# Performance work log

Measured on AMD Instinct MI355X. Metric: run time of the kernel, lower is better.

## Reference

```python
import jax, jax.numpy as jnp
import numpy as np


def setup_inputs() -> dict:
    key = jax.random.key(0)
    k1, k2 = jax.random.split(key)
    x = jax.random.normal(k1, (128, 256, 32, 32), dtype=jnp.float32)
    T = jax.random.randint(k2, (128, 256, 1, 1), 0, 2, dtype=jnp.int32)
    return {"x": x, "T": T, "drop_block": 5}


def reference(x, T, drop_block):
    b, c, h, w = x.shape
    n = b * c
    xf = x.reshape(n, h, w)
    sel = (T.reshape(n) != 0)

    # per-slice argmax location
    flat = xf.reshape(n, h * w)
    max_index = jnp.argmax(flat, axis=1)
    mh = max_index // w
    mw = max_index % w

    half = int(np.floor(drop_block / 2.0))  # floor(drop_block/2)
    h1 = jnp.clip(mh - half, 0, h - 1)
    h2 = jnp.clip(mh + half, 0, h - 1)
    w1 = jnp.clip(mw - half, 0, w - 1)
    w2 = jnp.clip(mw + half, 0, w - 1)

    rows = jnp.arange(h)  # [h]
    cols = jnp.arange(w)  # [w]
    in_rows = (rows[None, :] >= h1[:, None]) & (rows[None, :] <= h2[:, None])  # [n,h]
    in_cols = (cols[None, :] >= w1[:, None]) & (cols[None, :] <= w2[:, None])  # [n,w]
    in_box = in_rows[:, :, None] & in_cols[:, None, :]                          # [n,h,w]
    S = 1.0 - in_box.astype(x.dtype)

    # normalization so expected activation magnitude is preserved
    lam = (h * w) / jnp.sum(S, axis=(1, 2))  # [n]
    masked = xf * S * lam[:, None, None]

    out = jnp.where(sel[:, None, None], masked, xf)
    return out.reshape(b, c, h, w)
```

## Files before the change

### kernel.cpp

```cpp
#include <hip/hip_runtime.h>

typedef float nfloat4 __attribute__((ext_vector_type(4)));

__global__ __launch_bounds__(256) void drop_block_kernel(
    const float* __restrict__ x,
    const int* __restrict__ T,
    const int* __restrict__ dropb,
    float* __restrict__ out,
    int n_slices) {
  const int wave_in_blk = threadIdx.x >> 6;
  const int lane = threadIdx.x & 63;
  const int slice = blockIdx.x * 4 + wave_in_blk;
  if (slice >= n_slices) return;

  const nfloat4* __restrict__ x4 = (const nfloat4*)x + (size_t)slice * 256;
  nfloat4* __restrict__ o4 = (nfloat4*)out + (size_t)slice * 256;

  nfloat4 v0 = __builtin_nontemporal_load(&x4[lane]);
  nfloat4 v1 = __builtin_nontemporal_load(&x4[lane + 64]);
  nfloat4 v2 = __builtin_nontemporal_load(&x4[lane + 128]);
  nfloat4 v3 = __builtin_nontemporal_load(&x4[lane + 192]);

  const int sel = T[slice];

  if (!sel) {
    __builtin_nontemporal_store(v0, &o4[lane]);
    __builtin_nontemporal_store(v1, &o4[lane + 64]);
    __builtin_nontemporal_store(v2, &o4[lane + 128]);
    __builtin_nontemporal_store(v3, &o4[lane + 192]);
    return;
  }

#define ARG4(vec, base, BV, BI)                         \
  float BV = vec.x; int BI = (base);                    \
  if (vec.y > BV) { BV = vec.y; BI = (base) + 1; }      \
  if (vec.z > BV) { BV = vec.z; BI = (base) + 2; }      \
  if (vec.w > BV) { BV = vec.w; BI = (base) + 3; }

  ARG4(v0, lane * 4, bv0, bi0)
  ARG4(v1, (lane + 64) * 4, bv1, bi1)
  ARG4(v2, (lane + 128) * 4, bv2, bi2)
  ARG4(v3, (lane + 192) * 4, bv3, bi3)
#undef ARG4

  float bv = bv0; int bi = bi0;
  if (bv1 > bv) { bv = bv1; bi = bi1; }
  if (bv2 > bv) { bv = bv2; bi = bi2; }
  if (bv3 > bv) { bv = bv3; bi = bi3; }

  for (int off = 32; off > 0; off >>= 1) {
    float ov = __shfl_xor(bv, off, 64);
    int oi = __shfl_xor(bi, off, 64);
    if (ov > bv || (ov == bv && oi < bi)) { bv = ov; bi = oi; }
  }

  const int half = dropb[0] >> 1;
  const int mh = bi >> 5;
  const int mw = bi & 31;
  int h1 = mh - half; h1 = h1 < 0 ? 0 : (h1 > 31 ? 31 : h1);
  int h2 = mh + half; h2 = h2 < 0 ? 0 : (h2 > 31 ? 31 : h2);
  int w1 = mw - half; w1 = w1 < 0 ? 0 : (w1 > 31 ? 31 : w1);
  int w2 = mw + half; w2 = w2 < 0 ? 0 : (w2 > 31 ? 31 : w2);
  const int area = (h2 - h1 + 1) * (w2 - w1 + 1);
  const float lam = 1024.0f / (float)(1024 - area);

#define APPLY(vec, base)                                              \
  do {                                                                \
    nfloat4 _r;                                                       \
    {                                                                 \
      int _i = (base);                                                \
      int _r0 = _i >> 5, _c0 = _i & 31;                               \
      bool _in = (_r0 >= h1) & (_r0 <= h2) & (_c0 >= w1) & (_c0 <= w2); \
      _r.x = _in ? 0.0f : vec.x * lam;                                \
      _c0 = (_i + 1) & 31; _r0 = (_i + 1) >> 5;                       \
      _in = (_r0 >= h1) & (_r0 <= h2) & (_c0 >= w1) & (_c0 <= w2);    \
      _r.y = _in ? 0.0f : vec.y * lam;                                \
      _c0 = (_i + 2) & 31; _r0 = (_i + 2) >> 5;                       \
      _in = (_r0 >= h1) & (_r0 <= h2) & (_c0 >= w1) & (_c0 <= w2);    \
      _r.z = _in ? 0.0f : vec.z * lam;                                \
      _c0 = (_i + 3) & 31; _r0 = (_i + 3) >> 5;                       \
      _in = (_r0 >= h1) & (_r0 <= h2) & (_c0 >= w1) & (_c0 <= w2);    \
      _r.w = _in ? 0.0f : vec.w * lam;                                \
    }                                                                 \
    __builtin_nontemporal_store(_r, &o4[(base) >> 2]);                \
  } while (0)

  APPLY(v0, lane * 4);
  APPLY(v1, (lane + 64) * 4);
  APPLY(v2, (lane + 128) * 4);
  APPLY(v3, (lane + 192) * 4);
#undef APPLY
}

extern "C" void kernel_launch(void* const* d_in, const int* in_sizes, int n_in,
                              void* d_out, int out_size, void* d_ws, size_t ws_size,
                              hipStream_t stream) {
  const float* x = (const float*)d_in[0];
  const int* T = (const int*)d_in[1];
  const int* dropb = (const int*)d_in[2];
  float* out = (float*)d_out;

  const int n_slices = in_sizes[1];
  const int blocks = (n_slices + 3) / 4;
  drop_block_kernel<<<blocks, 256, 0, stream>>>(x, T, dropb, out, n_slices);
}
```

Before: 220.8 us.

## Process two slices per wave and remove the unselected-slice branch

Each wavefront now handles two 32x32 slices, issuing eight vector loads up front, and interleaves the two argmax reductions. The separate early-exit copy path for unselected slices is removed: those slices go through the masking code with an empty box and a scale of one. Selection flags and the block size are read through readfirstlane so they live in scalar registers. The aim is more memory-level parallelism per wave and half as many blocks, at the cost of more registers and doing argmax work on slices that only need a copy.

```diff
diff --git a/kernel.cpp b/kernel.cpp
--- a/kernel.cpp
+++ b/kernel.cpp
@@ -8,28 +8,34 @@
     const int* __restrict__ dropb,
     float* __restrict__ out,
     int n_slices) {
-  const int wave_in_blk = threadIdx.x >> 6;
+  const int wave = threadIdx.x >> 6;
   const int lane = threadIdx.x & 63;
-  const int slice = blockIdx.x * 4 + wave_in_blk;
-  if (slice >= n_slices) return;
+  const int s0 = blockIdx.x * 8 + wave * 2;
+  if (s0 >= n_slices) return;
+  const bool has_b = (s0 + 1) < n_slices;
 
-  const nfloat4* __restrict__ x4 = (const nfloat4*)x + (size_t)slice * 256;
-  nfloat4* __restrict__ o4 = (nfloat4*)out + (size_t)slice * 256;
+  const nfloat4* __restrict__ xa = (const nfloat4*)x + (size_t)s0 * 256;
+  nfloat4* __restrict__ oa = (nfloat4*)out + (size_t)s0 * 256;
+  const nfloat4* __restrict__ xb = xa + 256;
+  nfloat4* __restrict__ ob = oa + 256;
 
-  nfloat4 v0 = __builtin_nontemporal_load(&x4[lane]);
-  nfloat4 v1 = __builtin_nontemporal_load(&x4[lane + 64]);
-  nfloat4 v2 = __builtin_nontemporal_load(&x4[lane + 128]);
-  nfloat4 v3 = __builtin_nontemporal_load(&x4[lane + 192]);
+  nfloat4 a0 = __builtin_nontemporal_load(&xa[lane]);
+  nfloat4 a1 = __builtin_nontemporal_load(&xa[lane + 64]);
+  nfloat4 a2 = __builtin_nontemporal_load(&xa[lane + 128]);
+  nfloat4 a3 = __builtin_nontemporal_load(&xa[lane + 192]);
+  nfloat4 b0, b1, b2, b3;
+  if (has_b) {
+    b0 = __builtin_nontemporal_load(&xb[lane]);
+    b1 = __builtin_nontemporal_load(&xb[lane + 64]);
+    b2 = __builtin_nontemporal_load(&xb[lane + 128]);
+    b3 = __builtin_nontemporal_load(&xb[lane + 192]);
+  } else {
+    b0 = a0; b1 = a1; b2 = a2; b3 = a3;
+  }
 
-  const int sel = T[slice];
-
-  if (!sel) {
-    __builtin_nontemporal_store(v0, &o4[lane]);
-    __builtin_nontemporal_store(v1, &o4[lane + 64]);
-    __builtin_nontemporal_store(v2, &o4[lane + 128]);
-    __builtin_nontemporal_store(v3, &o4[lane + 192]);
-    return;
-  }
+  int sel_a = __builtin_amdgcn_readfirstlane(T[s0]);
+  int sel_b = has_b ? __builtin_amdgcn_readfirstlane(T[s0 + 1]) : 0;
+  const int half = __builtin_amdgcn_readfirstlane(dropb[0]) >> 1;
 
 #define ARG4(vec, base, BV, BI)                         \
   float BV = vec.x; int BI = (base);                    \
@@ -37,58 +43,82 @@
   if (vec.z > BV) { BV = vec.z; BI = (base) + 2; }      \
   if (vec.w > BV) { BV = vec.w; BI = (base) + 3; }
 
-  ARG4(v0, lane * 4, bv0, bi0)
-  ARG4(v1, (lane + 64) * 4, bv1, bi1)
-  ARG4(v2, (lane + 128) * 4, bv2, bi2)
-  ARG4(v3, (lane + 192) * 4, bv3, bi3)
+  ARG4(a0, lane * 4, av0, ai0)
+  ARG4(a1, (lane + 64) * 4, av1, ai1)
+  ARG4(a2, (lane + 128) * 4, av2, ai2)
+  ARG4(a3, (lane + 192) * 4, av3, ai3)
+  ARG4(b0, lane * 4, bv0, bi0)
+  ARG4(b1, (lane + 64) * 4, bv1, bi1)
+  ARG4(b2, (lane + 128) * 4, bv2, bi2)
+  ARG4(b3, (lane + 192) * 4, bv3, bi3)
 #undef ARG4
 
+  float av = av0; int ai = ai0;
+  if (av1 > av) { av = av1; ai = ai1; }
+  if (av2 > av) { av = av2; ai = ai2; }
+  if (av3 > av) { av = av3; ai = ai3; }
   float bv = bv0; int bi = bi0;
   if (bv1 > bv) { bv = bv1; bi = bi1; }
   if (bv2 > bv) { bv = bv2; bi = bi2; }
   if (bv3 > bv) { bv = bv3; bi = bi3; }
 
   for (int off = 32; off > 0; off >>= 1) {
-    float ov = __shfl_xor(bv, off, 64);
-    int oi = __shfl_xor(bi, off, 64);
-    if (ov > bv || (ov == bv && oi < bi)) { bv = ov; bi = oi; }
+    float oav = __shfl_xor(av, off, 64);
+    int oai = __shfl_xor(ai, off, 64);
+    float obv = __shfl_xor(bv, off, 64);
+    int obi = __shfl_xor(bi, off, 64);
+    if (oav > av || (oav == av && oai < ai)) { av = oav; ai = oai; }
+    if (obv > bv || (obv == bv && obi < bi)) { bv = obv; bi = obi; }
   }
 
-  const int half = dropb[0] >> 1;
-  const int mh = bi >> 5;
-  const int mw = bi & 31;
-  int h1 = mh - half; h1 = h1 < 0 ? 0 : (h1 > 31 ? 31 : h1);
-  int h2 = mh + half; h2 = h2 < 0 ? 0 : (h2 > 31 ? 31 : h2);
-  int w1 = mw - half; w1 = w1 < 0 ? 0 : (w1 > 31 ? 31 : w1);
-  int w2 = mw + half; w2 = w2 < 0 ? 0 : (w2 > 31 ? 31 : w2);
-  const int area = (h2 - h1 + 1) * (w2 - w1 + 1);
-  const float lam = 1024.0f / (float)(1024 - area);
+#define BOX(BI, SEL, H1, H2, W1, W2, LAM)                              \
+  int H1, H2, W1, W2; float LAM;                                       \
+  {                                                                    \
+    const int mh = (BI) >> 5, mw = (BI) & 31;                          \
+    int h1 = mh - half; h1 = h1 < 0 ? 0 : (h1 > 31 ? 31 : h1);         \
+    int h2 = mh + half; h2 = h2 < 0 ? 0 : (h2 > 31 ? 31 : h2);         \
+    int w1 = mw - half; w1 = w1 < 0 ? 0 : (w1 > 31 ? 31 : w1);         \
+    int w2 = mw + half; w2 = w2 < 0 ? 0 : (w2 > 31 ? 31 : w2);         \
+    const int area = (h2 - h1 + 1) * (w2 - w1 + 1);                    \
+    float lam = 1024.0f / (float)(1024 - area);                        \
+    H1 = (SEL) ? h1 : 32;                   \
+    H2 = h2; W1 = w1; W2 = w2;                                         \
+    LAM = (SEL) ? lam : 1.0f;                                          \
+  }
 
-#define APPLY(vec, base)                                              \
-  do {                                                                \
-    nfloat4 _r;                                                       \
-    {                                                                 \
-      int _i = (base);                                                \
-      int _r0 = _i >> 5, _c0 = _i & 31;                               \
-      bool _in = (_r0 >= h1) & (_r0 <= h2) & (_c0 >= w1) & (_c0 <= w2); \
-      _r.x = _in ? 0.0f : vec.x * lam;                                \
-      _c0 = (_i + 1) & 31; _r0 = (_i + 1) >> 5;                       \
-      _in = (_r0 >= h1) & (_r0 <= h2) & (_c0 >= w1) & (_c0 <= w2);    \
-      _r.y = _in ? 0.0f : vec.y * lam;                                \
-      _c0 = (_i + 2) & 31; _r0 = (_i + 2) >> 5;                       \
-      _in = (_r0 >= h1) & (_r0 <= h2) & (_c0 >= w1) & (_c0 <= w2);    \
-      _r.z = _in ? 0.0f : vec.z * lam;                                \
-      _c0 = (_i + 3) & 31; _r0 = (_i + 3) >> 5;                       \
-      _in = (_r0 >= h1) & (_r0 <= h2) & (_c0 >= w1) & (_c0 <= w2);    \
-      _r.w = _in ? 0.0f : vec.w * lam;                                \
-    }                                                                 \
-    __builtin_nontemporal_store(_r, &o4[(base) >> 2]);                \
+  BOX(ai, sel_a, ah1, ah2, aw1, aw2, alam)
+  BOX(bi, sel_b, bh1, bh2, bw1, bw2, blam)
+#undef BOX
+
+#define APPLY(vec, base, H1, H2, W1, W2, LAM, optr)                    \
+  do {                                                                 \
+    nfloat4 _r;                                                        \
+    int _i = (base);                                                   \
+    int _r0 = _i >> 5, _c0 = _i & 31;                                  \
+    bool _in = (_r0 >= H1) & (_r0 <= H2) & (_c0 >= W1) & (_c0 <= W2);  \
+    _r.x = _in ? 0.0f : vec.x * LAM;                                   \
+    _r0 = (_i + 1) >> 5; _c0 = (_i + 1) & 31;                          \
+    _in = (_r0 >= H1) & (_r0 <= H2) & (_c0 >= W1) & (_c0 <= W2);       \
+    _r.y = _in ? 0.0f : vec.y * LAM;                                   \
+    _r0 = (_i + 2) >> 5; _c0 = (_i + 2) & 31;                          \
+    _in = (_r0 >= H1) & (_r0 <= H2) & (_c0 >= W1) & (_c0 <= W2);       \
+    _r.z = _in ? 0.0f : vec.z * LAM;                                   \
+    _r0 = (_i + 3) >> 5; _c0 = (_i + 3) & 31;                          \
+    _in = (_r0 >= H1) & (_r0 <= H2) & (_c0 >= W1) & (_c0 <= W2);       \
+    _r.w = _in ? 0.0f : vec.w * LAM;                                   \
+    __builtin_nontemporal_store(_r, &(optr)[(base) >> 2]);             \
   } while (0)
 
-  APPLY(v0, lane * 4);
-  APPLY(v1, (lane + 64) * 4);
-  APPLY(v2, (lane + 128) * 4);
-  APPLY(v3, (lane + 192) * 4);
+  APPLY(a0, lane * 4, ah1, ah2, aw1, aw2, alam, oa);
+  APPLY(a1, (lane + 64) * 4, ah1, ah2, aw1, aw2, alam, oa);
+  APPLY(a2, (lane + 128) * 4, ah1, ah2, aw1, aw2, alam, oa);
+  APPLY(a3, (lane + 192) * 4, ah1, ah2, aw1, aw2, alam, oa);
+  if (has_b) {
+    APPLY(b0, lane * 4, bh1, bh2, bw1, bw2, blam, ob);
+    APPLY(b1, (lane + 64) * 4, bh1, bh2, bw1, bw2, blam, ob);
+    APPLY(b2, (lane + 128) * 4, bh1, bh2, bw1, bw2, blam, ob);
+    APPLY(b3, (lane + 192) * 4, bh1, bh2, bw1, bw2, blam, ob);
+  }
 #undef APPLY
 }
 
@@ -101,6 +131,6 @@
   float* out = (float*)d_out;
 
   const int n_slices = in_sizes[1];
-  const int blocks = (n_slices + 3) / 4;
+  const int blocks = (n_slices + 7) / 8;
   drop_block_kernel<<<blocks, 256, 0, stream>>>(x, T, dropb, out, n_slices);
 }
```

Result: no change. 223.3 us (+1.1%).
